# Optimization experiments

Measured on AMD Instinct MI355X. Metric: run time of the kernel, lower is better.

Reference implementation:

```python
import jax, jax.numpy as jnp
import numpy as np

B, L, IN_DIM, D_MODEL = 4, 1024, 128, 256
MDIM = 2 * D_MODEL          # mamba_dim = 512 (must equal 2*d_model for shape consistency)
NL = 4                      # mamba_layers
DIN = 2 * MDIM              # d_inner (expand=2)
NST = 16                    # d_state
DTR = MDIM // 16            # dt_rank = 32
KC = 4                      # d_conv
EPS = 1e-5

# sinusoidal positional encoding buffer (deterministic)
_pos = np.arange(L, dtype=np.float32)[:, None]
_div = np.exp(np.arange(0, MDIM, 2, dtype=np.float32) * (-np.log(10000.0) / MDIM))
_pe = np.zeros((L, MDIM), dtype=np.float32)
_pe[:, 0::2] = np.sin(_pos * _div)
_pe[:, 1::2] = np.cos(_pos * _div)
PE = jnp.asarray(_pe)


def setup_inputs() -> dict:
    key = jax.random.key(0)
    ks = iter(jax.random.split(key, 64))
    rn = lambda shape, s=0.02: jax.random.normal(next(ks), shape, jnp.float32) * s
    inp = {
        "x": jax.random.normal(next(ks), (B, L, IN_DIM), jnp.float32),
        "rtg": jax.random.normal(next(ks), (B, L, 1), jnp.float32),
        "state_emb_w": rn((D_MODEL, IN_DIM)), "state_emb_b": jnp.zeros((D_MODEL,)),
        "reward_emb_w": rn((D_MODEL, 1)), "reward_emb_b": jnp.zeros((D_MODEL,)),
        "ln_w": jnp.ones((MDIM,)), "ln_b": jnp.zeros((MDIM,)),
        "in_proj_w": rn((NL, 2 * DIN, MDIM)),
        "conv_w": rn((NL, DIN, KC), 0.1), "conv_b": jnp.zeros((NL, DIN)),
        "x_proj_w": rn((NL, DTR + 2 * NST, DIN)),
        "dt_proj_w": rn((NL, DIN, DTR), 0.1), "dt_proj_b": jnp.full((NL, DIN), -2.0),
        "A_log": jnp.tile(jnp.log(jnp.arange(1, NST + 1, dtype=jnp.float32)), (NL, DIN, 1)),
        "D_param": jnp.ones((NL, DIN)),
        "out_proj_w": rn((NL, MDIM, DIN)),
        "norm_w": jnp.ones((NL, MDIM)), "norm_f_w": jnp.ones((MDIM,)),
        "so_w1": rn((MDIM // 2, MDIM)), "so_b1": jnp.zeros((MDIM // 2,)),
        "so_w2": rn((IN_DIM, MDIM // 2)), "so_b2": jnp.zeros((IN_DIM,)),
        "ro_w1": rn((MDIM // 2, MDIM)), "ro_b1": jnp.zeros((MDIM // 2,)),
        "ro_w2": rn((1, MDIM // 2)), "ro_b2": jnp.zeros((1,)),
    }
    return inp


def _rmsnorm(h, w):
    return h * jax.lax.rsqrt(jnp.mean(h * h, -1, keepdims=True) + EPS) * w


def _mamba(h, ipw, cw, cb, xpw, dpw, dpb, Alog, Dp, opw):
    # h: [B,L,MDIM]
    Ls = h.shape[1]
    xz = h @ ipw.T                                   # [B,L,2*DIN]
    xx, z = jnp.split(xz, 2, axis=-1)
    # causal depthwise conv, kernel KC, left pad KC-1
    xp = jnp.pad(xx, ((0, 0), (KC - 1, 0), (0, 0)))
    xc = cb + sum(cw[:, k] * xp[:, k:k + Ls, :] for k in range(KC))
    xc = jax.nn.silu(xc)                             # [B,L,DIN]
    dbc = xc @ xpw.T                                 # [B,L,DTR+2*NST]
    dt = jax.nn.softplus(dbc[..., :DTR] @ dpw.T + dpb)   # [B,L,DIN]
    Bm = dbc[..., DTR:DTR + NST]                     # [B,L,NST]
    Cm = dbc[..., DTR + NST:]                        # [B,L,NST]
    A = -jnp.exp(Alog)                               # [DIN,NST]

    def step(hc, inp):
        dt_t, B_t, C_t, x_t = inp                    # [B,DIN],[B,NST],[B,NST],[B,DIN]
        hc = jnp.exp(dt_t[:, :, None] * A) * hc + (dt_t * x_t)[:, :, None] * B_t[:, None, :]
        return hc, jnp.einsum('bdn,bn->bd', hc, C_t)

    h0 = jnp.zeros((h.shape[0], DIN, NST), h.dtype)
    _, ys = jax.lax.scan(step, h0, (dt.swapaxes(0, 1), Bm.swapaxes(0, 1),
                                    Cm.swapaxes(0, 1), xc.swapaxes(0, 1)))
    y = ys.swapaxes(0, 1) + Dp * xc
    y = y * jax.nn.silu(z)
    return y @ opw.T                                 # [B,L,MDIM]


def _forward(x, rtg, state_emb_w, state_emb_b, reward_emb_w, reward_emb_b, ln_w, ln_b,
             in_proj_w, conv_w, conv_b, x_proj_w, dt_proj_w, dt_proj_b, A_log, D_param,
             out_proj_w, norm_w, norm_f_w, so_w1, so_b1, so_w2, so_b2, ro_w1, ro_b1, ro_w2, ro_b2):
    se = x @ state_emb_w.T + state_emb_b            # [B,L,D_MODEL]
    re = rtg @ reward_emb_w.T + reward_emb_b        # [B,L,D_MODEL]
    h = jnp.concatenate([se, re], axis=-1)          # [B,L,MDIM]
    h = h + PE[:h.shape[1]]                          # dropout is identity at eval
    mu = jnp.mean(h, -1, keepdims=True)
    var = jnp.var(h, -1, keepdims=True)
    h = (h - mu) * jax.lax.rsqrt(var + EPS) * ln_w + ln_b
    residual = None
    for i in range(NL):
        residual = h if residual is None else h + residual
        hn = _rmsnorm(residual, norm_w[i])
        h = _mamba(hn, in_proj_w[i], conv_w[i], conv_b[i], x_proj_w[i],
                   dt_proj_w[i], dt_proj_b[i], A_log[i], D_param[i], out_proj_w[i])
    residual = h + residual
    h = _rmsnorm(residual, norm_f_w)
    next_state = jax.nn.relu(h @ so_w1.T + so_b1) @ so_w2.T + so_b2   # [B,L,IN_DIM]
    next_reward = jax.nn.relu(h @ ro_w1.T + ro_b1) @ ro_w2.T + ro_b2  # [B,L,1]
    return next_state, next_reward


def reference(x, rtg, state_emb_w, state_emb_b, reward_emb_w, reward_emb_b, ln_w, ln_b,
              in_proj_w, conv_w, conv_b, x_proj_w, dt_proj_w, dt_proj_b, A_log, D_param,
              out_proj_w, norm_w, norm_f_w, so_w1, so_b1, so_w2, so_b2, ro_w1, ro_b1, ro_w2, ro_b2):
    return _forward(x, rtg, state_emb_w, state_emb_b, reward_emb_w, reward_emb_b, ln_w, ln_b,
                    in_proj_w, conv_w, conv_b, x_proj_w, dt_proj_w, dt_proj_b, A_log, D_param,
                    out_proj_w, norm_w, norm_f_w, so_w1, so_b1, so_w2, so_b2, ro_w1, ro_b1, ro_w2, ro_b2)
```

## Files before the change

### kernel.cpp

```cpp
#include <hip/hip_runtime.h>
#include <stdint.h>

typedef unsigned short u16;
typedef __attribute__((ext_vector_type(8))) short bf16x8;
typedef __attribute__((ext_vector_type(4))) float f32x4;

static __device__ __forceinline__ u16 f2b(float f) {
  uint32_t u = __builtin_bit_cast(uint32_t, f);
  u += 0x7fffu + ((u >> 16) & 1u);
  return (u16)(u >> 16);
}
static __device__ __forceinline__ float b2f(u16 h) {
  uint32_t u = ((uint32_t)h) << 16;
  return __builtin_bit_cast(float, u);
}

#define GLDS16(gsrc, ldst)                                                        \
  __builtin_amdgcn_global_load_lds(                                               \
      (const __attribute__((address_space(1))) void*)(gsrc),                      \
      (__attribute__((address_space(3))) void*)(ldst), 16, 0, 0)

__global__ void f2b_kernel(const float* __restrict__ in, u16* __restrict__ out, int n) {
  int i = blockIdx.x * 256 + threadIdx.x;
  if (i < n) out[i] = f2b(in[i]);
}

__global__ __launch_bounds__(256) void pe_kernel(float* __restrict__ PEt) {
  const int l = blockIdx.x;
  const float c = -9.210340371976184f / 512.f;
#pragma unroll
  for (int q = 0; q < 2; ++q) {
    int dd = threadIdx.x + q * 256;
    float div = expf((float)(2 * (dd >> 1)) * c);
    float v = (dd & 1) ? cosf((float)l * div) : sinf((float)l * div);
    PEt[(size_t)l * 512 + dd] = v;
  }
}

__global__ __launch_bounds__(256) void dpw_t_kernel(const float* __restrict__ dpw,
                                                    float* __restrict__ dpwT) {
  const int l = blockIdx.y;
  int idx = blockIdx.x * 256 + threadIdx.x;
  int j = idx >> 10, dd = idx & 1023;
  dpwT[(size_t)l * 32768 + idx] = dpw[(size_t)l * 32768 + (size_t)dd * 32 + j];
}

__global__ __launch_bounds__(256) void embed_ln2(
    const float* __restrict__ x, const float* __restrict__ rtg,
    const float* __restrict__ Wse, const float* __restrict__ bse,
    const float* __restrict__ Wre, const float* __restrict__ bre,
    const float* __restrict__ lnw, const float* __restrict__ lnb,
    const float* __restrict__ PEt, float* __restrict__ h) {
  const int tid = threadIdx.x;
  const int tok0 = blockIdx.x * 16;
  const int l0 = tok0 & 1023;
  __shared__ float xs[16][128];
  __shared__ float rt[16];
  __shared__ float sw[16][2][4];
  for (int i = tid; i < 16 * 128; i += 256) ((float*)xs)[i] = x[(size_t)tok0 * 128 + i];
  if (tid < 16) rt[tid] = rtg[tok0 + tid];
  __syncthreads();
  const int d = tid;
  float acc[16];
#pragma unroll
  for (int tt = 0; tt < 16; ++tt) acc[tt] = 0.f;
  const float* wrow = Wse + (size_t)d * 128;
  for (int k0 = 0; k0 < 128; k0 += 8) {
    float4 wa = *(const float4*)(wrow + k0);
    float4 wb = *(const float4*)(wrow + k0 + 4);
#pragma unroll
    for (int tt = 0; tt < 16; ++tt) {
      const float* xr = &xs[tt][k0];
      acc[tt] += xr[0] * wa.x + xr[1] * wa.y + xr[2] * wa.z + xr[3] * wa.w +
                 xr[4] * wb.x + xr[5] * wb.y + xr[6] * wb.z + xr[7] * wb.w;
    }
  }
  const float seb = bse[d], reW = Wre[d], reB = bre[d];
  const int lane = tid & 63, wv = tid >> 6;
  float h1a[16];
#pragma unroll
  for (int tt = 0; tt < 16; ++tt) {
    float h0 = acc[tt] + seb + PEt[(size_t)(l0 + tt) * 512 + d];
    float h1 = reB + rt[tt] * reW + PEt[(size_t)(l0 + tt) * 512 + 256 + d];
    acc[tt] = h0;
    h1a[tt] = h1;
    float s = h0 + h1, q = h0 * h0 + h1 * h1;
#pragma unroll
    for (int o = 32; o; o >>= 1) { s += __shfl_xor(s, o); q += __shfl_xor(q, o); }
    if (lane == 0) { sw[tt][0][wv] = s; sw[tt][1][wv] = q; }
  }
  __syncthreads();
#pragma unroll
  for (int tt = 0; tt < 16; ++tt) {
    float S = sw[tt][0][0] + sw[tt][0][1] + sw[tt][0][2] + sw[tt][0][3];
    float Q = sw[tt][1][0] + sw[tt][1][1] + sw[tt][1][2] + sw[tt][1][3];
    float mean = S * (1.f / 512.f);
    float var = Q * (1.f / 512.f) - mean * mean;
    float rstd = rsqrtf(var + 1e-5f);
    size_t base = (size_t)(tok0 + tt) * 512;
    h[base + d]       = (acc[tt] - mean) * rstd * lnw[d] + lnb[d];
    h[base + 256 + d] = (h1a[tt] - mean) * rstd * lnw[256 + d] + lnb[256 + d];
  }
}

__global__ __launch_bounds__(256) void resid_rms_kernel(
    const float* __restrict__ hin, float* __restrict__ residual,
    const float* __restrict__ w, u16* __restrict__ outb, int first) {
  const int tok = blockIdx.x;
  const int t = threadIdx.x;
  __shared__ float rq[4];
  size_t base = (size_t)tok * 512;
  float v0 = hin[base + t], v1 = hin[base + t + 256];
  if (!first) { v0 += residual[base + t]; v1 += residual[base + t + 256]; }
  residual[base + t] = v0;
  residual[base + t + 256] = v1;
  float q = v0 * v0 + v1 * v1;
#pragma unroll
  for (int o = 32; o; o >>= 1) q += __shfl_xor(q, o);
  if ((t & 63) == 0) rq[t >> 6] = q;
  __syncthreads();
  float Q = rq[0] + rq[1] + rq[2] + rq[3];
  float scale = rsqrtf(Q * (1.f / 512.f) + 1e-5f);
  outb[base + t]       = f2b(v0 * scale * w[t]);
  outb[base + t + 256] = f2b(v1 * scale * w[t + 256]);
}

template <int BM, int BN, int WM, int WN, int EPI>
__global__ __launch_bounds__(256) void gemm_bt(
    const u16* __restrict__ A, const u16* __restrict__ Bw,
    float* __restrict__ Cf, u16* __restrict__ Cb,
    const float* __restrict__ bias, int M, int N, int K) {
  constexpr int MF = BM / (WM * 16);
  constexpr int NF = BN / (WN * 16);
  constexpr int NCA = (BM * 4) / 256;
  constexpr int NCB = (BN * 4) / 256;
  __shared__ __align__(16) u16 lA[BM * 32];
  __shared__ __align__(16) u16 lB[BN * 32];
  const int tid = threadIdx.x;
  const int lane = tid & 63;
  const int wv = tid >> 6;
  const int wr = wv / WN, wc = wv % WN;
  const int m0 = blockIdx.x * BM, n0 = blockIdx.y * BN;
  const int kchunk = K / gridDim.z;
  const int kb = blockIdx.z * kchunk;

  f32x4 acc[MF][NF];
#pragma unroll
  for (int i = 0; i < MF; ++i)
#pragma unroll
    for (int j = 0; j < NF; ++j) acc[i][j] = (f32x4){0.f, 0.f, 0.f, 0.f};

  const int srow = tid >> 2, sck = tid & 3;
  const u16* Ag = A + (size_t)(m0 + srow) * K + sck * 8 + kb;
  const u16* Bg = Bw + (size_t)(n0 + srow) * K + sck * 8 + kb;

  for (int k0 = 0; k0 < kchunk; k0 += 32) {
#pragma unroll
    for (int it = 0; it < NCA; ++it)
      GLDS16(Ag + (size_t)it * 64 * K + k0, &lA[(it * 256 + tid) * 8]);
#pragma unroll
    for (int it = 0; it < NCB; ++it)
      GLDS16(Bg + (size_t)it * 64 * K + k0, &lB[(it * 256 + tid) * 8]);
    __syncthreads();
    bf16x8 af[MF], bfr[NF];
    const int koff = (lane >> 4) * 8;
#pragma unroll
    for (int mi = 0; mi < MF; ++mi) {
      int r = wr * (MF * 16) + mi * 16 + (lane & 15);
      af[mi] = *(const bf16x8*)(&lA[r * 32 + koff]);
    }
#pragma unroll
    for (int ni = 0; ni < NF; ++ni) {
      int r = wc * (NF * 16) + ni * 16 + (lane & 15);
      bfr[ni] = *(const bf16x8*)(&lB[r * 32 + koff]);
    }
#pragma unroll
    for (int mi = 0; mi < MF; ++mi)
#pragma unroll
      for (int ni = 0; ni < NF; ++ni)
        acc[mi][ni] = __builtin_amdgcn_mfma_f32_16x16x32_bf16(af[mi], bfr[ni], acc[mi][ni], 0, 0, 0);
    __syncthreads();
  }

  float* co = Cf + (size_t)blockIdx.z * (size_t)M * N;
  const int rbase = (lane >> 4) * 4;
  const int cbase = lane & 15;
#pragma unroll
  for (int mi = 0; mi < MF; ++mi) {
#pragma unroll
    for (int ni = 0; ni < NF; ++ni) {
      int row = m0 + wr * (MF * 16) + mi * 16 + rbase;
      int col = n0 + wc * (NF * 16) + ni * 16 + cbase;
      float bv = (EPI >= 2) ? bias[col] : 0.f;
#pragma unroll
      for (int r = 0; r < 4; ++r) {
        float v = acc[mi][ni][r] + bv;
        if (EPI == 2) v = fmaxf(v, 0.f);
        size_t idx = (size_t)(row + r) * N + col;
        if (EPI == 1 || EPI == 2) Cb[idx] = f2b(v);
        else co[idx] = v;
      }
    }
  }
}

__global__ __launch_bounds__(256) void conv_silu_kernel(
    const u16* __restrict__ xz, const float* __restrict__ cw,
    const float* __restrict__ cb, float* __restrict__ xc, u16* __restrict__ xcb) {
  int idx = blockIdx.x * 256 + threadIdx.x;
  int d = idx & 1023;
  int t = (idx >> 10) & 1023;
  int token = idx >> 10;
  float4 w4 = *(const float4*)(cw + (size_t)d * 4);
  const float wk[4] = {w4.x, w4.y, w4.z, w4.w};
  float s = cb[d];
  const u16* xx = xz + (size_t)(token - t) * 2048 + d;
#pragma unroll
  for (int k = 0; k < 4; ++k) {
    int tt = t - 3 + k;
    if (tt >= 0) s += wk[k] * b2f(xx[(size_t)tt * 2048]);
  }
  float sl = s / (1.f + expf(-s));
  xc[idx] = sl;
  xcb[idx] = f2b(sl);
}

__global__ __launch_bounds__(256) void dt_kernel2(
    const float* __restrict__ P, const float* __restrict__ dpwT,
    const float* __restrict__ dpb, float* __restrict__ dtout,
    float* __restrict__ dbcr) {
  const int tid = threadIdx.x;
  const int tok0 = blockIdx.x * 16;
  __shared__ float sm[16][64];
  const size_t str = (size_t)4096 * 64;
  for (int i = tid; i < 16 * 64; i += 256) {
    size_t o = (size_t)tok0 * 64 + i;
    float v = P[o] + P[str + o] + P[2 * str + o] + P[3 * str + o];
    ((float*)sm)[i] = v;
    dbcr[o] = v;
  }
  __syncthreads();
  float acc0[16], acc1[16], acc2[16], acc3[16];
#pragma unroll
  for (int t = 0; t < 16; ++t) { acc0[t] = 0.f; acc1[t] = 0.f; acc2[t] = 0.f; acc3[t] = 0.f; }
#pragma unroll 4
  for (int j = 0; j < 32; ++j) {
    float w0 = dpwT[(size_t)j * 1024 + tid];
    float w1 = dpwT[(size_t)j * 1024 + 256 + tid];
    float w2 = dpwT[(size_t)j * 1024 + 512 + tid];
    float w3 = dpwT[(size_t)j * 1024 + 768 + tid];
#pragma unroll
    for (int t = 0; t < 16; ++t) {
      float sv = sm[t][j];
      acc0[t] += sv * w0;
      acc1[t] += sv * w1;
      acc2[t] += sv * w2;
      acc3[t] += sv * w3;
    }
  }
  const float b0 = dpb[tid], b1 = dpb[256 + tid], b2 = dpb[512 + tid], b3 = dpb[768 + tid];
#pragma unroll
  for (int t = 0; t < 16; ++t) {
    size_t o = (size_t)(tok0 + t) * 1024 + tid;
    float a0 = acc0[t] + b0, a1 = acc1[t] + b1, a2 = acc2[t] + b2, a3 = acc3[t] + b3;
    dtout[o]       = (a0 > 20.f) ? a0 : logf(1.f + expf(a0));
    dtout[o + 256] = (a1 > 20.f) ? a1 : logf(1.f + expf(a1));
    dtout[o + 512] = (a2 > 20.f) ? a2 : logf(1.f + expf(a2));
    dtout[o + 768] = (a3 > 20.f) ? a3 : logf(1.f + expf(a3));
  }
}

__global__ __launch_bounds__(256) void scan1(
    const float* __restrict__ dt, const float* __restrict__ xc,
    const float* __restrict__ dbc, const float* __restrict__ Alog,
    float* __restrict__ Ebuf, float* __restrict__ Ubuf, int NCc, int TCc) {
  const int d = blockIdx.x * 256 + threadIdx.x;
  const int c = blockIdx.y;
  const int b = blockIdx.z;
  const int t0 = c * TCc;
  __shared__ __align__(16) float sB[64][16];
  for (int i = threadIdx.x; i < TCc * 16; i += 256) {
    int t = i >> 4, n = i & 15;
    sB[t][n] = dbc[((size_t)(b * 1024 + t0 + t)) * 64 + 32 + n];
  }
  float A2[16];
#pragma unroll
  for (int q = 0; q < 4; ++q) {
    float4 a4 = *(const float4*)(Alog + (size_t)d * 16 + q * 4);
    A2[q * 4 + 0] = -expf(a4.x) * 1.4426950408889634f;
    A2[q * 4 + 1] = -expf(a4.y) * 1.4426950408889634f;
    A2[q * 4 + 2] = -expf(a4.z) * 1.4426950408889634f;
    A2[q * 4 + 3] = -expf(a4.w) * 1.4426950408889634f;
  }
  __syncthreads();
  float hc[16];
#pragma unroll
  for (int n = 0; n < 16; ++n) hc[n] = 0.f;
  float sumdt = 0.f;
  size_t tok = (size_t)b * 1024 + t0;
  for (int t = 0; t < TCc; ++t, ++tok) {
    float dtv = dt[tok * 1024 + d];
    float xcv = xc[tok * 1024 + d];
    float du = dtv * xcv;
    sumdt += dtv;
#pragma unroll
    for (int q = 0; q < 4; ++q) {
      float4 B4 = *(const float4*)(&sB[t][q * 4]);
      float e0 = exp2f(dtv * A2[q * 4 + 0]);
      float e1 = exp2f(dtv * A2[q * 4 + 1]);
      float e2 = exp2f(dtv * A2[q * 4 + 2]);
      float e3 = exp2f(dtv * A2[q * 4 + 3]);
      hc[q * 4 + 0] = e0 * hc[q * 4 + 0] + du * B4.x;
      hc[q * 4 + 1] = e1 * hc[q * 4 + 1] + du * B4.y;
      hc[q * 4 + 2] = e2 * hc[q * 4 + 2] + du * B4.z;
      hc[q * 4 + 3] = e3 * hc[q * 4 + 3] + du * B4.w;
    }
  }
  size_t ob = (((size_t)b * NCc + c) * 16) * 1024 + d;
#pragma unroll
  for (int n = 0; n < 16; ++n) {
    Ebuf[ob + (size_t)n * 1024] = exp2f(A2[n] * sumdt);
    Ubuf[ob + (size_t)n * 1024] = hc[n];
  }
}

__global__ __launch_bounds__(256) void scan2(
    const float* __restrict__ dt, const float* __restrict__ xc,
    const float* __restrict__ dbc, const u16* __restrict__ xz,
    const float* __restrict__ Alog, const float* __restrict__ Dp,
    const float* __restrict__ Ebuf, const float* __restrict__ Ubuf,
    u16* __restrict__ yg, int NCc, int TCc) {
  const int d = blockIdx.x * 256 + threadIdx.x;
  const int c = blockIdx.y;
  const int b = blockIdx.z;
  const int t0 = c * TCc;
  __shared__ __align__(16) float sB[64][16];
  __shared__ __align__(16) float sC[64][16];
  for (int i = threadIdx.x; i < TCc * 16; i += 256) {
    int t = i >> 4, n = i & 15;
    size_t o = ((size_t)(b * 1024 + t0 + t)) * 64 + 32;
    sB[t][n] = dbc[o + n];
    sC[t][n] = dbc[o + 16 + n];
  }
  float A2[16];
#pragma unroll
  for (int q = 0; q < 4; ++q) {
    float4 a4 = *(const float4*)(Alog + (size_t)d * 16 + q * 4);
    A2[q * 4 + 0] = -expf(a4.x) * 1.4426950408889634f;
    A2[q * 4 + 1] = -expf(a4.y) * 1.4426950408889634f;
    A2[q * 4 + 2] = -expf(a4.z) * 1.4426950408889634f;
    A2[q * 4 + 3] = -expf(a4.w) * 1.4426950408889634f;
  }
  const float Dd = Dp[d];
  float hc[16];
#pragma unroll
  for (int n = 0; n < 16; ++n) hc[n] = 0.f;
  for (int cc = 0; cc < c; ++cc) {
    size_t ob = (((size_t)b * NCc + cc) * 16) * 1024 + d;
#pragma unroll
    for (int n = 0; n < 16; ++n)
      hc[n] = Ebuf[ob + (size_t)n * 1024] * hc[n] + Ubuf[ob + (size_t)n * 1024];
  }
  __syncthreads();
  size_t tok = (size_t)b * 1024 + t0;
  for (int t = 0; t < TCc; ++t, ++tok) {
    float dtv = dt[tok * 1024 + d];
    float xcv = xc[tok * 1024 + d];
    float du = dtv * xcv;
    float y0 = 0.f, y1 = 0.f, y2 = 0.f, y3 = 0.f;
#pragma unroll
    for (int q = 0; q < 4; ++q) {
      float4 B4 = *(const float4*)(&sB[t][q * 4]);
      float4 C4 = *(const float4*)(&sC[t][q * 4]);
      float e0 = exp2f(dtv * A2[q * 4 + 0]);
      float e1 = exp2f(dtv * A2[q * 4 + 1]);
      float e2 = exp2f(dtv * A2[q * 4 + 2]);
      float e3 = exp2f(dtv * A2[q * 4 + 3]);
      hc[q * 4 + 0] = e0 * hc[q * 4 + 0] + du * B4.x;
      hc[q * 4 + 1] = e1 * hc[q * 4 + 1] + du * B4.y;
      hc[q * 4 + 2] = e2 * hc[q * 4 + 2] + du * B4.z;
      hc[q * 4 + 3] = e3 * hc[q * 4 + 3] + du * B4.w;
      y0 += hc[q * 4 + 0] * C4.x;
      y1 += hc[q * 4 + 1] * C4.y;
      y2 += hc[q * 4 + 2] * C4.z;
      y3 += hc[q * 4 + 3] * C4.w;
    }
    float y = (y0 + y1) + (y2 + y3);
    float z = b2f(xz[tok * 2048 + 1024 + d]);
    float g = z / (1.f + expf(-z));
    yg[tok * 1024 + d] = f2b((y + Dd * xcv) * g);
  }
}

__global__ __launch_bounds__(256) void reward_head_kernel(
    const u16* __restrict__ t1r, const float* __restrict__ w2,
    const float* __restrict__ b2, float* __restrict__ outr) {
  int tok = blockIdx.x * 4 + (threadIdx.x >> 6);
  int lane = threadIdx.x & 63;
  float s = 0.f;
#pragma unroll
  for (int j = 0; j < 256; j += 64) s += b2f(t1r[(size_t)tok * 256 + j + lane]) * w2[j + lane];
#pragma unroll
  for (int o = 32; o; o >>= 1) s += __shfl_xor(s, o);
  if (lane == 0) outr[tok] = s + b2[0];
}

extern "C" void kernel_launch(void* const* d_in, const int* in_sizes, int n_in,
                              void* d_out, int out_size, void* d_ws, size_t ws_size,
                              hipStream_t stream) {
  const float* x    = (const float*)d_in[0];
  const float* rtg  = (const float*)d_in[1];
  const float* Wse  = (const float*)d_in[2];
  const float* bse  = (const float*)d_in[3];
  const float* Wre  = (const float*)d_in[4];
  const float* bre  = (const float*)d_in[5];
  const float* lnw  = (const float*)d_in[6];
  const float* lnb  = (const float*)d_in[7];
  const float* ipw  = (const float*)d_in[8];
  const float* cw   = (const float*)d_in[9];
  const float* cb   = (const float*)d_in[10];
  const float* xpw  = (const float*)d_in[11];
  const float* dpw  = (const float*)d_in[12];
  const float* dpb  = (const float*)d_in[13];
  const float* Alog = (const float*)d_in[14];
  const float* Dp   = (const float*)d_in[15];
  const float* opw  = (const float*)d_in[16];
  const float* nw   = (const float*)d_in[17];
  const float* nfw  = (const float*)d_in[18];
  const float* sow1 = (const float*)d_in[19];
  const float* sob1 = (const float*)d_in[20];
  const float* sow2 = (const float*)d_in[21];
  const float* sob2 = (const float*)d_in[22];
  const float* row1 = (const float*)d_in[23];
  const float* rob1 = (const float*)d_in[24];
  const float* row2 = (const float*)d_in[25];
  const float* rob2 = (const float*)d_in[26];
  (void)in_sizes; (void)n_in; (void)out_size;

  char* wsp = (char*)d_ws;
  size_t off = 0;
  auto alloc = [&](size_t bytes) -> void* {
    off = (off + 255) & ~(size_t)255;
    void* p = wsp + off;
    off += bytes;
    return p;
  };
  const int TOK = 4096;
  float* h     = (float*)alloc((size_t)TOK * 512 * 4);
  float* resid = (float*)alloc((size_t)TOK * 512 * 4);
  u16* hn      = (u16*)alloc((size_t)TOK * 512 * 2);
  u16* xzb     = (u16*)alloc((size_t)TOK * 2048 * 2);
  float* xcf   = (float*)alloc((size_t)TOK * 1024 * 4);
  u16* xcb     = (u16*)alloc((size_t)TOK * 1024 * 2);
  float* dbcP  = (float*)alloc((size_t)4 * TOK * 64 * 4);
  float* dbc   = (float*)alloc((size_t)TOK * 64 * 4);
  float* dtf   = (float*)alloc((size_t)TOK * 1024 * 4);
  float* PEt   = (float*)alloc((size_t)1024 * 512 * 4);
  float* dpwT  = (float*)alloc((size_t)4 * 32 * 1024 * 4);
  u16* ipwb    = (u16*)alloc((size_t)4 * 2048 * 512 * 2);
  u16* xpwb    = (u16*)alloc((size_t)4 * 64 * 1024 * 2);
  u16* opwb    = (u16*)alloc((size_t)4 * 512 * 1024 * 2);
  u16* sow1b   = (u16*)alloc((size_t)256 * 512 * 2);
  u16* sow2b   = (u16*)alloc((size_t)128 * 256 * 2);
  u16* row1b   = (u16*)alloc((size_t)256 * 512 * 2);

  size_t base_off = (off + 255) & ~(size_t)255;
  int NCc = (ws_size >= base_off + (size_t)2 * 4096 * 32 * 16 * 4 + 4096) ? 32 : 16;
  int TCc = 1024 / NCc;
  char* shared8 = (char*)alloc((size_t)2 * 4096 * NCc * 16 * 4);
  float* Ebuf  = (float*)shared8;
  float* Ubuf  = Ebuf + (size_t)4096 * NCc * 16;
  u16* t1s     = (u16*)shared8;
  u16* t1r     = t1s + (size_t)TOK * 256;

  auto cvt = [&](const float* src, u16* dst, int n) {
    f2b_kernel<<<(n + 255) / 256, 256, 0, stream>>>(src, dst, n);
  };
  cvt(ipw, ipwb, 4 * 2048 * 512);
  cvt(xpw, xpwb, 4 * 64 * 1024);
  cvt(opw, opwb, 4 * 512 * 1024);
  cvt(sow1, sow1b, 256 * 512);
  cvt(sow2, sow2b, 128 * 256);
  cvt(row1, row1b, 256 * 512);

  pe_kernel<<<1024, 256, 0, stream>>>(PEt);
  dpw_t_kernel<<<dim3(128, 4), 256, 0, stream>>>(dpw, dpwT);
  embed_ln2<<<256, 256, 0, stream>>>(x, rtg, Wse, bse, Wre, bre, lnw, lnb, PEt, h);

  for (int i = 0; i < 4; ++i) {
    resid_rms_kernel<<<TOK, 256, 0, stream>>>(h, resid, nw + i * 512, hn, i == 0);
    gemm_bt<128, 128, 2, 2, 1><<<dim3(32, 16, 1), 256, 0, stream>>>(
        hn, ipwb + (size_t)i * 2048 * 512, nullptr, xzb, nullptr, 4096, 2048, 512);
    conv_silu_kernel<<<TOK * 1024 / 256, 256, 0, stream>>>(
        xzb, cw + (size_t)i * 4096, cb + i * 1024, xcf, xcb);
    gemm_bt<128, 64, 2, 2, 0><<<dim3(32, 1, 4), 256, 0, stream>>>(
        xcb, xpwb + (size_t)i * 64 * 1024, dbcP, nullptr, nullptr, 4096, 64, 1024);
    dt_kernel2<<<TOK / 16, 256, 0, stream>>>(dbcP, dpwT + (size_t)i * 32 * 1024,
                                             dpb + i * 1024, dtf, dbc);
    scan1<<<dim3(4, NCc - 1, 4), 256, 0, stream>>>(
        dtf, xcf, dbc, Alog + (size_t)i * 1024 * 16, Ebuf, Ubuf, NCc, TCc);
    scan2<<<dim3(4, NCc, 4), 256, 0, stream>>>(
        dtf, xcf, dbc, xzb, Alog + (size_t)i * 1024 * 16, Dp + i * 1024,
        Ebuf, Ubuf, xcb, NCc, TCc);
    gemm_bt<128, 64, 2, 2, 0><<<dim3(32, 8, 1), 256, 0, stream>>>(
        xcb, opwb + (size_t)i * 512 * 1024, h, nullptr, nullptr, 4096, 512, 1024);
  }

  resid_rms_kernel<<<TOK, 256, 0, stream>>>(h, resid, nfw, hn, 0);
  gemm_bt<64, 64, 2, 2, 2><<<dim3(64, 4, 1), 256, 0, stream>>>(
      hn, sow1b, nullptr, t1s, sob1, 4096, 256, 512);
  gemm_bt<64, 64, 2, 2, 3><<<dim3(64, 2, 1), 256, 0, stream>>>(
      t1s, sow2b, (float*)d_out, nullptr, sob2, 4096, 128, 256);
  gemm_bt<64, 64, 2, 2, 2><<<dim3(64, 4, 1), 256, 0, stream>>>(
      hn, row1b, nullptr, t1r, rob1, 4096, 256, 512);
  reward_head_kernel<<<TOK / 4, 256, 0, stream>>>(
      t1r, row2, rob2, (float*)d_out + (size_t)TOK * 128);
}
```

Measured before the change: 730.7 us.

## Add separate chunk-carry scan kernel and allow more scan chunks

Adds a scan_mid kernel that computes each chunk's starting state once with a sequential pass over chunks per (batch, state, channel). scan2 now reads that precomputed initial state instead of each block re-combining all earlier chunks, which cost work quadratic in the chunk count. This makes a finer chunking (64 chunks) affordable when workspace allows, giving more parallel blocks in scan1/scan2. The cost is an extra kernel launch, an extra H0 buffer and its memory traffic.

```diff
diff --git a/kernel.cpp b/kernel.cpp
--- a/kernel.cpp
+++ b/kernel.cpp
@@ -324,12 +324,27 @@
   }
 }
 
+__global__ __launch_bounds__(256) void scan_mid(
+    const float* __restrict__ Ebuf, const float* __restrict__ Ubuf,
+    float* __restrict__ H0, int NCc) {
+  int idx = blockIdx.x * 256 + threadIdx.x;
+  int b = idx >> 14;
+  int nd = idx & 16383;
+  float h = 0.f;
+  size_t o0 = ((size_t)b * NCc * 16) * 1024 + nd;
+  const size_t cstr = (size_t)16 * 1024;
+  for (int cc = 0; cc < NCc; ++cc) {
+    size_t o = o0 + (size_t)cc * cstr;
+    H0[o] = h;
+    if (cc < NCc - 1) h = Ebuf[o] * h + Ubuf[o];
+  }
+}
+
 __global__ __launch_bounds__(256) void scan2(
     const float* __restrict__ dt, const float* __restrict__ xc,
     const float* __restrict__ dbc, const u16* __restrict__ xz,
     const float* __restrict__ Alog, const float* __restrict__ Dp,
-    const float* __restrict__ Ebuf, const float* __restrict__ Ubuf,
-    u16* __restrict__ yg, int NCc, int TCc) {
+    const float* __restrict__ H0, u16* __restrict__ yg, int NCc, int TCc) {
   const int d = blockIdx.x * 256 + threadIdx.x;
   const int c = blockIdx.y;
   const int b = blockIdx.z;
@@ -353,14 +368,9 @@
   }
   const float Dd = Dp[d];
   float hc[16];
-#pragma unroll
-  for (int n = 0; n < 16; ++n) hc[n] = 0.f;
-  for (int cc = 0; cc < c; ++cc) {
-    size_t ob = (((size_t)b * NCc + cc) * 16) * 1024 + d;
-#pragma unroll
-    for (int n = 0; n < 16; ++n)
-      hc[n] = Ebuf[ob + (size_t)n * 1024] * hc[n] + Ubuf[ob + (size_t)n * 1024];
-  }
+  size_t ob = (((size_t)b * NCc + c) * 16) * 1024 + d;
+#pragma unroll
+  for (int n = 0; n < 16; ++n) hc[n] = H0[ob + (size_t)n * 1024];
   __syncthreads();
   size_t tok = (size_t)b * 1024 + t0;
   for (int t = 0; t < TCc; ++t, ++tok) {
@@ -465,11 +475,17 @@
   u16* row1b   = (u16*)alloc((size_t)256 * 512 * 2);
 
   size_t base_off = (off + 255) & ~(size_t)255;
-  int NCc = (ws_size >= base_off + (size_t)2 * 4096 * 32 * 16 * 4 + 4096) ? 32 : 16;
+  auto scan_bytes = [](int nc) {
+    return (size_t)3 * 4 * nc * 16 * 1024 * 4 + 512;
+  };
+  int NCc = 16;
+  if (ws_size >= base_off + scan_bytes(64)) NCc = 64;
+  else if (ws_size >= base_off + scan_bytes(32)) NCc = 32;
   int TCc = 1024 / NCc;
   char* shared8 = (char*)alloc((size_t)2 * 4096 * NCc * 16 * 4);
   float* Ebuf  = (float*)shared8;
   float* Ubuf  = Ebuf + (size_t)4096 * NCc * 16;
+  float* H0    = (float*)alloc((size_t)4096 * NCc * 16 * 4);
   u16* t1s     = (u16*)shared8;
   u16* t1r     = t1s + (size_t)TOK * 256;
 
@@ -499,9 +515,10 @@
                                              dpb + i * 1024, dtf, dbc);
     scan1<<<dim3(4, NCc - 1, 4), 256, 0, stream>>>(
         dtf, xcf, dbc, Alog + (size_t)i * 1024 * 16, Ebuf, Ubuf, NCc, TCc);
+    scan_mid<<<256, 256, 0, stream>>>(Ebuf, Ubuf, H0, NCc);
     scan2<<<dim3(4, NCc, 4), 256, 0, stream>>>(
         dtf, xcf, dbc, xzb, Alog + (size_t)i * 1024 * 16, Dp + i * 1024,
-        Ebuf, Ubuf, xcb, NCc, TCc);
+        H0, xcb, NCc, TCc);
     gemm_bt<128, 64, 2, 2, 0><<<dim3(32, 8, 1), 256, 0, stream>>>(
         xcb, opwb + (size_t)i * 512 * 1024, h, nullptr, nullptr, 4096, 512, 1024);
   }
```

Result: no change. 721.0 us (-1.3%).
